# Kernel optimization log

Measured on AMD Instinct MI355X. Metric: run time of the kernel, lower is better.

## Reference

```python
import jax, jax.numpy as jnp
import numpy as np

EPS = 1e-05


def setup_inputs() -> dict:
    key = jax.random.key(0)
    k1, _ = jax.random.split(key)
    x = jax.random.normal(k1, (4, 8192, 1024), dtype=jnp.float32)
    weight = jnp.ones((1024,), dtype=jnp.float32)
    return {"x": x, "weight": weight}


def reference(x, weight):
    # GMRNorm, elementwise=True path. The original computes, per channel c,
    # mean[b,t,c] = sum_{s<=t} x[b,s,c] / (t+1) via a [T,T] triangular matmul,
    # with the (0,0) entry zeroed so mean at t=0 is 0. This is exactly a
    # cumulative sum divided by the prefix count, computed here in O(B*T*C).
    x = x.astype(jnp.float32)
    B, T, C = x.shape
    counts = jnp.arange(1, T + 1, dtype=jnp.float32)[:, None]  # [T,1]
    mean = jnp.cumsum(x, axis=1) / counts                      # [B,T,C]
    mean = mean.at[:, 0, :].set(0.0)                           # causal_matrix[0,0] = 0
    xc = x - mean
    norm_x = jnp.mean(xc * xc, axis=-1, keepdims=True)         # per-timestep variance over C
    x_normed = xc * jax.lax.rsqrt(norm_x + EPS)
    return weight * x_normed
```

## Files before the change

kernel.cpp:

```cpp
#include <hip/hip_runtime.h>

#define T_    8192
#define C_    1024
#define TCH   8
#define NCH   (T_ / TCH)
#define SBS   32
#define NSB   (NCH / SBS)

__global__ __launch_bounds__(256) void k_chunk_sums(const float* __restrict__ x,
                                                    float* __restrict__ S) {
    const int ch = blockIdx.x;
    const int b  = blockIdx.y;
    const int c  = threadIdx.x * 4;
    const float* xp = x + ((size_t)(b * T_ + ch * TCH) * C_ + c);
    float4 s = make_float4(0.f, 0.f, 0.f, 0.f);
#pragma unroll
    for (int i = 0; i < TCH; ++i) {
        float4 v = *(const float4*)(xp + (size_t)i * C_);
        s.x += v.x; s.y += v.y; s.z += v.z; s.w += v.w;
    }
    *(float4*)(S + ((size_t)(b * NCH + ch) * C_ + c)) = s;
}

__global__ __launch_bounds__(256) void k_scan_a(float* __restrict__ S,
                                                float* __restrict__ S2) {
    const int idx = blockIdx.x * 256 + threadIdx.x;
    const int c   = idx & (C_ - 1);
    const int sb  = (idx >> 10) & (NSB - 1);
    const int b   = idx >> 15;
    float* p = S + ((size_t)(b * NCH + sb * SBS) * C_ + c);
    float run = 0.f;
#pragma unroll 4
    for (int j = 0; j < SBS; ++j) {
        float v = p[(size_t)j * C_];
        p[(size_t)j * C_] = run;
        run += v;
    }
    S2[(size_t)(b * NSB + sb) * C_ + c] = run;
}

__global__ __launch_bounds__(256) void k_scan_b(float* __restrict__ S2) {
    const int idx = blockIdx.x * 256 + threadIdx.x;
    const int c = idx & (C_ - 1);
    const int b = idx >> 10;
    float* p = S2 + ((size_t)b * NSB * C_ + c);
    float run = 0.f;
#pragma unroll 4
    for (int j = 0; j < NSB; ++j) {
        float v = p[(size_t)j * C_];
        p[(size_t)j * C_] = run;
        run += v;
    }
}

__global__ __launch_bounds__(256) void k_norm(const float* __restrict__ x,
                                              const float* __restrict__ S,
                                              const float* __restrict__ S2,
                                              const float* __restrict__ w,
                                              float* __restrict__ out) {
    const int wave = threadIdx.x >> 6;
    const int lane = threadIdx.x & 63;
    const int ch   = blockIdx.x * 4 + wave;
    const int b    = blockIdx.y;
    const int cb   = lane * 4;

    float4 run[4], wt[4];
    const float* Pp  = S  + (size_t)(b * NCH + ch) * C_;
    const float* P2p = S2 + (size_t)(b * NSB + (ch / SBS)) * C_;
#pragma unroll
    for (int q = 0; q < 4; ++q) {
        float4 a  = *(const float4*)(Pp  + q * 256 + cb);
        float4 bb = *(const float4*)(P2p + q * 256 + cb);
        run[q] = make_float4(a.x + bb.x, a.y + bb.y, a.z + bb.z, a.w + bb.w);
        wt[q]  = *(const float4*)(w + q * 256 + cb);
    }

    const int t0 = ch * TCH;
    const float* xp = x   + (size_t)(b * T_ + t0) * C_;
    float*       op = out + (size_t)(b * T_ + t0) * C_;
    const float invC = 1.0f / (float)C_;

#pragma unroll
    for (int i = 0; i < TCH; ++i) {
        const int t = t0 + i;
        float4 xv[4];
#pragma unroll
        for (int q = 0; q < 4; ++q)
            xv[q] = *(const float4*)(xp + (size_t)i * C_ + q * 256 + cb);

        const float m = (t == 0) ? 0.0f : 1.0f / (float)(t + 1);

        float4 xc[4];
        float sq = 0.f;
#pragma unroll
        for (int q = 0; q < 4; ++q) {
            run[q].x += xv[q].x;  xc[q].x = xv[q].x - run[q].x * m;  sq += xc[q].x * xc[q].x;
            run[q].y += xv[q].y;  xc[q].y = xv[q].y - run[q].y * m;  sq += xc[q].y * xc[q].y;
            run[q].z += xv[q].z;  xc[q].z = xv[q].z - run[q].z * m;  sq += xc[q].z * xc[q].z;
            run[q].w += xv[q].w;  xc[q].w = xv[q].w - run[q].w * m;  sq += xc[q].w * xc[q].w;
        }

#pragma unroll
        for (int off = 32; off; off >>= 1)
            sq += __shfl_xor(sq, off, 64);

        const float scale = rsqrtf(sq * invC + 1e-5f);

#pragma unroll
        for (int q = 0; q < 4; ++q) {
            float4 o;
            o.x = wt[q].x * xc[q].x * scale;
            o.y = wt[q].y * xc[q].y * scale;
            o.z = wt[q].z * xc[q].z * scale;
            o.w = wt[q].w * xc[q].w * scale;
            *(float4*)(op + (size_t)i * C_ + q * 256 + cb) = o;
        }
    }
}

extern "C" void kernel_launch(void* const* d_in, const int* in_sizes, int n_in,
                              void* d_out, int out_size, void* d_ws, size_t ws_size,
                              hipStream_t stream) {
    const float* x = (const float*)d_in[0];
    const float* w = (const float*)d_in[1];
    float* out = (float*)d_out;

    const int B = in_sizes[0] / (T_ * C_);

    float* S  = (float*)d_ws;
    float* S2 = S + (size_t)B * NCH * C_;

    dim3 g1(NCH, B);
    k_chunk_sums<<<g1, 256, 0, stream>>>(x, S);

    const int na = B * NSB * C_;
    k_scan_a<<<na / 256, 256, 0, stream>>>(S, S2);

    const int nb = B * C_;
    k_scan_b<<<nb / 256, 256, 0, stream>>>(S2);

    dim3 g2(NCH / 4, B);
    k_norm<<<g2, 256, 0, stream>>>(x, S, S2, w, out);
}
```

Before: 265.6 us.

## Fuse chunk sums with local scan and batch row reductions in norm kernel

Merges the chunk-sum kernel and the first scan kernel into a single kernel in which each block sums 8 chunks of 8 rows and writes exclusive prefixes directly, removing one launch and a full read-modify-write pass over the chunk-sum buffer. The superblock size shrinks from 32 to 8, so the second-level scan gets longer and the first kernel's grid smaller. The norm kernel now handles 4 timesteps per batch, interleaving their wave shuffle reductions for more ILP. It also uses fast hardware rcp/rsq intrinsics and a 3-blocks-per-SIMD launch bound, at the cost of more registers per thread and slightly lower precision.

```diff
diff --git a/kernel.cpp b/kernel.cpp
--- a/kernel.cpp
+++ b/kernel.cpp
@@ -4,39 +4,32 @@
 #define C_    1024
 #define TCH   8
 #define NCH   (T_ / TCH)
-#define SBS   32
+#define SBS   8
 #define NSB   (NCH / SBS)
+#define BATCH 4
 
-__global__ __launch_bounds__(256) void k_chunk_sums(const float* __restrict__ x,
-                                                    float* __restrict__ S) {
-    const int ch = blockIdx.x;
+__global__ __launch_bounds__(256) void k_sumscan(const float* __restrict__ x,
+                                                 float* __restrict__ S,
+                                                 float* __restrict__ S2) {
+    const int sb = blockIdx.x;
     const int b  = blockIdx.y;
     const int c  = threadIdx.x * 4;
-    const float* xp = x + ((size_t)(b * T_ + ch * TCH) * C_ + c);
-    float4 s = make_float4(0.f, 0.f, 0.f, 0.f);
+    const float* xp = x + ((size_t)(b * T_ + sb * SBS * TCH) * C_ + c);
+    float* Sp = S + ((size_t)(b * NCH + sb * SBS) * C_ + c);
+    float4 run = make_float4(0.f, 0.f, 0.f, 0.f);
 #pragma unroll
-    for (int i = 0; i < TCH; ++i) {
-        float4 v = *(const float4*)(xp + (size_t)i * C_);
-        s.x += v.x; s.y += v.y; s.z += v.z; s.w += v.w;
+    for (int j = 0; j < SBS; ++j) {
+        *(float4*)(Sp + (size_t)j * C_) = run;
+        float4 v[TCH];
+#pragma unroll
+        for (int i = 0; i < TCH; ++i)
+            v[i] = *(const float4*)(xp + (size_t)(j * TCH + i) * C_);
+#pragma unroll
+        for (int i = 0; i < TCH; ++i) {
+            run.x += v[i].x; run.y += v[i].y; run.z += v[i].z; run.w += v[i].w;
+        }
     }
-    *(float4*)(S + ((size_t)(b * NCH + ch) * C_ + c)) = s;
-}
-
-__global__ __launch_bounds__(256) void k_scan_a(float* __restrict__ S,
-                                                float* __restrict__ S2) {
-    const int idx = blockIdx.x * 256 + threadIdx.x;
-    const int c   = idx & (C_ - 1);
-    const int sb  = (idx >> 10) & (NSB - 1);
-    const int b   = idx >> 15;
-    float* p = S + ((size_t)(b * NCH + sb * SBS) * C_ + c);
-    float run = 0.f;
-#pragma unroll 4
-    for (int j = 0; j < SBS; ++j) {
-        float v = p[(size_t)j * C_];
-        p[(size_t)j * C_] = run;
-        run += v;
-    }
-    S2[(size_t)(b * NSB + sb) * C_ + c] = run;
+    *(float4*)(S2 + ((size_t)(b * NSB + sb) * C_ + c)) = run;
 }
 
 __global__ __launch_bounds__(256) void k_scan_b(float* __restrict__ S2) {
@@ -45,7 +38,7 @@
     const int b = idx >> 10;
     float* p = S2 + ((size_t)b * NSB * C_ + c);
     float run = 0.f;
-#pragma unroll 4
+#pragma unroll 8
     for (int j = 0; j < NSB; ++j) {
         float v = p[(size_t)j * C_];
         p[(size_t)j * C_] = run;
@@ -53,11 +46,11 @@
     }
 }
 
-__global__ __launch_bounds__(256) void k_norm(const float* __restrict__ x,
-                                              const float* __restrict__ S,
-                                              const float* __restrict__ S2,
-                                              const float* __restrict__ w,
-                                              float* __restrict__ out) {
+__global__ __launch_bounds__(256, 3) void k_norm(const float* __restrict__ x,
+                                                 const float* __restrict__ S,
+                                                 const float* __restrict__ S2,
+                                                 const float* __restrict__ w,
+                                                 float* __restrict__ out) {
     const int wave = threadIdx.x >> 6;
     const int lane = threadIdx.x & 63;
     const int ch   = blockIdx.x * 4 + wave;
@@ -81,39 +74,52 @@
     const float invC = 1.0f / (float)C_;
 
 #pragma unroll
-    for (int i = 0; i < TCH; ++i) {
-        const int t = t0 + i;
-        float4 xv[4];
+    for (int h = 0; h < TCH / BATCH; ++h) {
+        float4 xc[BATCH][4];
+        float  sq[BATCH];
+
 #pragma unroll
-        for (int q = 0; q < 4; ++q)
-            xv[q] = *(const float4*)(xp + (size_t)i * C_ + q * 256 + cb);
-
-        const float m = (t == 0) ? 0.0f : 1.0f / (float)(t + 1);
-
-        float4 xc[4];
-        float sq = 0.f;
+        for (int i = 0; i < BATCH; ++i) {
+            const int tt = t0 + h * BATCH + i;
+            const float m = (tt == 0) ? 0.0f
+                                      : __builtin_amdgcn_rcpf((float)(tt + 1));
+            float s = 0.f;
 #pragma unroll
-        for (int q = 0; q < 4; ++q) {
-            run[q].x += xv[q].x;  xc[q].x = xv[q].x - run[q].x * m;  sq += xc[q].x * xc[q].x;
-            run[q].y += xv[q].y;  xc[q].y = xv[q].y - run[q].y * m;  sq += xc[q].y * xc[q].y;
-            run[q].z += xv[q].z;  xc[q].z = xv[q].z - run[q].z * m;  sq += xc[q].z * xc[q].z;
-            run[q].w += xv[q].w;  xc[q].w = xv[q].w - run[q].w * m;  sq += xc[q].w * xc[q].w;
+            for (int q = 0; q < 4; ++q) {
+                float4 v = *(const float4*)(xp + (size_t)(h * BATCH + i) * C_
+                                               + q * 256 + cb);
+                run[q].x += v.x; float a0 = v.x - run[q].x * m; s += a0 * a0;
+                run[q].y += v.y; float a1 = v.y - run[q].y * m; s += a1 * a1;
+                run[q].z += v.z; float a2 = v.z - run[q].z * m; s += a2 * a2;
+                run[q].w += v.w; float a3 = v.w - run[q].w * m; s += a3 * a3;
+                xc[i][q] = make_float4(a0, a1, a2, a3);
+            }
+            sq[i] = s;
         }
 
 #pragma unroll
-        for (int off = 32; off; off >>= 1)
-            sq += __shfl_xor(sq, off, 64);
+        for (int off = 32; off; off >>= 1) {
+#pragma unroll
+            for (int i = 0; i < BATCH; ++i)
+                sq[i] += __shfl_xor(sq[i], off, 64);
+        }
 
-        const float scale = rsqrtf(sq * invC + 1e-5f);
+        float scale[BATCH];
+#pragma unroll
+        for (int i = 0; i < BATCH; ++i)
+            scale[i] = __builtin_amdgcn_rsqf(sq[i] * invC + 1e-5f);
 
 #pragma unroll
-        for (int q = 0; q < 4; ++q) {
-            float4 o;
-            o.x = wt[q].x * xc[q].x * scale;
-            o.y = wt[q].y * xc[q].y * scale;
-            o.z = wt[q].z * xc[q].z * scale;
-            o.w = wt[q].w * xc[q].w * scale;
-            *(float4*)(op + (size_t)i * C_ + q * 256 + cb) = o;
+        for (int i = 0; i < BATCH; ++i) {
+#pragma unroll
+            for (int q = 0; q < 4; ++q) {
+                float4 o;
+                o.x = wt[q].x * xc[i][q].x * scale[i];
+                o.y = wt[q].y * xc[i][q].y * scale[i];
+                o.z = wt[q].z * xc[i][q].z * scale[i];
+                o.w = wt[q].w * xc[i][q].w * scale[i];
+                *(float4*)(op + (size_t)(h * BATCH + i) * C_ + q * 256 + cb) = o;
+            }
         }
     }
 }
@@ -130,11 +136,8 @@
     float* S  = (float*)d_ws;
     float* S2 = S + (size_t)B * NCH * C_;
 
-    dim3 g1(NCH, B);
-    k_chunk_sums<<<g1, 256, 0, stream>>>(x, S);
-
-    const int na = B * NSB * C_;
-    k_scan_a<<<na / 256, 256, 0, stream>>>(S, S2);
+    dim3 g1(NSB, B);
+    k_sumscan<<<g1, 256, 0, stream>>>(x, S, S2);
 
     const int nb = B * C_;
     k_scan_b<<<nb / 256, 256, 0, stream>>>(S2);
```

Result: no change. 267.1 us (+0.6%).
